# Performance work log

Measured on AMD Instinct MI355X. Metric: run time of the kernel, lower is better.

## Reference

```python
import jax, jax.numpy as jnp
import numpy as np

FRAME_LENGTH = 64
ATTENUATE_GAIN = 0.01


def setup_inputs() -> dict:
    key = jax.random.key(0)
    k1, k2 = jax.random.split(key)
    B, F, FC = 32, 4000, 65
    H = jax.random.uniform(k1, (B, F, FC), dtype=jnp.float32)
    noise = jax.random.uniform(k2, (B, F, FRAME_LENGTH), dtype=jnp.float32)
    return {"H": H, "noise": noise}


def reference(H, noise):
    B, F, fc = H.shape
    M = 2 * fc - 1                      # linear-phase IR length (129)
    L = M + FRAME_LENGTH - 1            # FFT conv length (192)

    # periodic hann window, matching torch.hann_window default
    win = 0.5 * (1.0 - jnp.cos(2.0 * jnp.pi * jnp.arange(M, dtype=jnp.float32) / M))

    # zero-phase FR -> zero-phase IR -> linear-phase windowed IR
    ir = jnp.fft.irfft(H.astype(jnp.complex64), n=M, axis=-1)  # (B, F, M)
    ir = jnp.roll(ir, fc - 1, axis=-1) * win

    # FFT-domain filtering (rfft with n=L zero-pads, same as explicit pad)
    IR = jnp.fft.rfft(ir, n=L, axis=-1)                        # (B, F, L//2+1)
    N = jnp.fft.rfft(noise * 2.0 - 1.0, n=L, axis=-1)          # (B, F, L//2+1)
    X = N * IR

    # Faithful to the original: irfft with n = number of BINS (97), which
    # trims the spectrum to n//2+1 bins and outputs n time samples.
    nb = X.shape[-1]                                           # 97
    y = jnp.fft.irfft(X, n=nb, axis=-1) * ATTENUATE_GAIN       # (B, F, nb)

    # overlap-add (equivalent to conv_transpose1d with identity kernel, stride=frame_length)
    out_len = (F - 1) * FRAME_LENGTH + nb
    idx = jnp.arange(F)[:, None] * FRAME_LENGTH + jnp.arange(nb)[None, :]  # (F, nb)
    out = jnp.zeros((B, out_len), dtype=y.dtype).at[:, idx].add(y)
    return out
```

## Files before the change

### kernel.cpp

```cpp
#include <hip/hip_runtime.h>
#include <math.h>

#define FC     65
#define NB     97
#define FRAME  64
#define B_     32
#define F_     4000
#define OUT_LEN ((F_ - 1) * FRAME + NB)
#define CHUNK  63
#define NCHUNK 64
#define ST     64
#define MROW   160

#define KP     128
#define D_ROW0 0
#define W_ROW0 64
#define E_ROW0 129
#define NROWS  226
#define GUARD_IDX (NROWS * KP)
#define MAGIC  0x5F3C0FEE

__global__ void fn_init(float* __restrict__ ws, int useGuard) {
    if (useGuard && ((const int*)ws)[GUARD_IDX] == MAGIC) return;
    int tid = blockIdx.x * blockDim.x + threadIdx.x;
    if (tid >= NROWS * KP) return;
    int row = tid >> 7;
    int fo  = tid & 127;
    int s   = fo >> 4;
    int w   = fo & 15;
    int slot = w >> 1, im = w & 1;
    int cnt  = (s == 0) ? 7 : 6;
    float val = 0.0f;
    if (slot < cnt) {
        int k = (s == 0) ? slot : (6 * s + 1 + slot);
        if (row < 64) {
            int j = row;
            double x = -(double)(k * j) / 96.0;
            val = im ? (float)sinpi(x) : (float)cospi(x);
        } else if (row < 129) {
            int kap = row - 64;
            double sr_ = cospi(-(double)k / 96.0), si_ = sinpi(-(double)k / 96.0);
            double er = 1.0, ei = 0.0;
            double C2 = 2.0 * cospi(2.0 * (double)kap / 129.0);
            double c_prev = cospi(-130.0 * (double)kap / 129.0);
            double c_cur  = cospi(-128.0 * (double)kap / 129.0);
            double U2 = 2.0 * cospi(2.0 / 129.0);
            double u_prev = cospi(2.0 / 129.0);
            double u_cur  = 1.0;
            double accr = 0.0, acci = 0.0;
            for (int m = 0; m < 129; m++) {
                double win = 0.5 * (1.0 - u_cur);
                double a = win * (1.0 / 129.0);
                if (kap) a *= 2.0 * c_cur;
                accr += a * er; acci += a * ei;
                double un = U2 * u_cur - u_prev; u_prev = u_cur; u_cur = un;
                double cn = C2 * c_cur - c_prev; c_prev = c_cur; c_cur = cn;
                double e2r = er * sr_ - ei * si_;
                double e2i = er * si_ + ei * sr_;
                er = e2r; ei = e2i;
            }
            val = im ? (float)acci : (float)accr;
        } else {
            int t = row - 129;
            double g = 0.01 / 97.0;
            double x = 2.0 * (double)(k * t) / 97.0;
            val = im ? (float)(k == 0 ? 0.0 : -2.0 * g * sinpi(x))
                     : (float)(g * (k == 0 ? 1.0 : 2.0) * cospi(x));
        }
    }
    ws[tid] = val;
}

__global__ void fn_seal(float* __restrict__ ws) { ((int*)ws)[GUARD_IDX] = MAGIC; }

__device__ __forceinline__ float dppx1(float x) {
    return __int_as_float(__builtin_amdgcn_mov_dpp(__float_as_int(x), 0xB1, 0xF, 0xF, false));
}
__device__ __forceinline__ float dppx2(float x) {
    return __int_as_float(__builtin_amdgcn_mov_dpp(__float_as_int(x), 0x4E, 0xF, 0xF, false));
}
__device__ __forceinline__ float dpphm(float x) {
    return __int_as_float(__builtin_amdgcn_mov_dpp(__float_as_int(x), 0x141, 0xF, 0xF, false));
}

#define FR4(M) M(0) M(1) M(2) M(3)

#define DXS(f,s) float Xr##f##_##s = 0.f, Xi##f##_##s = 0.f;
#define DXF(f) DXS(f,0) DXS(f,1) DXS(f,2) DXS(f,3) DXS(f,4) DXS(f,5) DXS(f,6)

#define P1S(f,nf,re,im,s) Xr##f##_##s = fmaf(nf,re,Xr##f##_##s); Xi##f##_##s = fmaf(nf,im,Xi##f##_##s);
#define P1F(f,nf,A,B,C,D) P1S(f,nf,A.x,A.y,0) P1S(f,nf,A.z,A.w,1) P1S(f,nf,B.x,B.y,2) \
  P1S(f,nf,B.z,B.w,3) P1S(f,nf,C.x,C.y,4) P1S(f,nf,C.z,C.w,5) P1S(f,nf,D.x,D.y,6)
#define P1ROW(A,B,C,D,na) P1F(0,na.x,A,B,C,D) P1F(1,na.y,A,B,C,D) P1F(2,na.z,A,B,C,D) P1F(3,na.w,A,B,C,D)

#define P3S(f,hf,re,im,s) Rr##f##_##s = fmaf(hf,re,Rr##f##_##s); Ri##f##_##s = fmaf(hf,im,Ri##f##_##s);
#define P3FA(f,hf,A,B) P3S(f,hf,A.x,A.y,0) P3S(f,hf,A.z,A.w,1) P3S(f,hf,B.x,B.y,2) P3S(f,hf,B.z,B.w,3)
#define P3ROWA(A,B,ha) P3FA(0,ha.x,A,B) P3FA(1,ha.y,A,B) P3FA(2,ha.z,A,B) P3FA(3,ha.w,A,B)
#define P3FB(f,hf,C,D) P3S(f,hf,C.x,C.y,4) P3S(f,hf,C.z,C.w,5) P3S(f,hf,D.x,D.y,6)
#define P3ROWB(C,D,ha) P3FB(0,ha.x,C,D) P3FB(1,ha.y,C,D) P3FB(2,ha.z,C,D) P3FB(3,ha.w,C,D)

#define P4S(f,s) { float xr_ = Xr##f##_##s*Rr##f##_##s - Xi##f##_##s*Ri##f##_##s; \
  Xi##f##_##s = Xr##f##_##s*Ri##f##_##s + Xi##f##_##s*Rr##f##_##s; Xr##f##_##s = xr_; }
#define P4FA(f) P4S(f,0) P4S(f,1) P4S(f,2) P4S(f,3)
#define P4FB(f) P4S(f,4) P4S(f,5) P4S(f,6)

#define P5S(f,re,im,s) y##f = fmaf(Xr##f##_##s,re,y##f); y##f = fmaf(Xi##f##_##s,im,y##f);
#define P5F(f,A,B,C,D) P5S(f,A.x,A.y,0) P5S(f,A.z,A.w,1) P5S(f,B.x,B.y,2) P5S(f,B.z,B.w,3) \
  P5S(f,C.x,C.y,4) P5S(f,C.z,C.w,5) P5S(f,D.x,D.y,6)
#define P5ROW(A,B,C,D) P5F(0,A,B,C,D) P5F(1,A,B,C,D) P5F(2,A,B,C,D) P5F(3,A,B,C,D)

#define P5REDUCE \
    float m0 = y0 + dpphm(y0); \
    float m1 = y1 + dpphm(y1); \
    float m2 = y2 + dpphm(y2); \
    float m3 = y3 + dpphm(y3); \
    float n0, n1, ym; \
    { float a_=(kg&2)?m2:m0, b_=(kg&2)?m0:m2; n0 = a_ + dppx2(b_); } \
    { float a_=(kg&2)?m3:m1, b_=(kg&2)?m1:m3; n1 = a_ + dppx2(b_); } \
    { float a_=(kg&1)?n1:n0, b_=(kg&1)?n0:n1; ym = a_ + dppx1(b_); }

#define OLAH(t_) if (kg < 4 && so) buf[(so - 1) * 65 + (t_)] = ym;
#define OLAT(t_) if (kg < 4) { int rr = (t_) - 64; \
    if (so < 63) buf[so * 65 + rr] += ym; \
    if (isLast) out[lastBase + (t_)] = ym; }

__launch_bounds__(128, 2)
__global__ void fn_main_kernel(const float* __restrict__ H,
                               const float* __restrict__ noise,
                               const float* __restrict__ ws,
                               float* __restrict__ out) {
    __shared__ __align__(16) float buf[65 * ST];
    __shared__ __align__(16) float lmat[4 * MROW];

    int bid = blockIdx.x;
    int b = bid >> 6;
    int c = bid & 63;
    int f0 = c * CHUNK;
    int nf = (CHUNK < F_ - f0) ? CHUNK : (F_ - f0);
    int T  = threadIdx.x;
    int wv = T >> 6;
    int L  = T & 63;
    int kg = L & 7;
    int fs = 32 * wv + 4 * (L >> 3);
    int so = fs + kg;
    int isLast = (kg < 4) && (f0 - 1 + so == F_ - 1);
    long lastBase = (long)b * OUT_LEN + (long)(F_ - 1) * FRAME;

    int srow = T >> 5;
    int sidx = T & 31;
    const float4* wsm = (const float4*)ws;
    float4* lput = (float4*)lmat + srow * 40 + (sidx >> 2) * 5 + (sidx & 3);
    const float4* lget = (const float4*)lmat + kg * 5;

    {
        int slot = T >> 1, half = T & 1;
        long nbase = ((long)b * F_ + (f0 - 1)) * FRAME + (long)slot * FRAME + half * 32;
        const long nmax = (long)B_ * F_ * FRAME - 4;
#pragma unroll 1
        for (int s4 = 0; s4 < 8; s4++) {
            long g = nbase + 4 * s4;
            g = g < 0 ? 0 : (g > nmax ? nmax : g);
            float4 v = *(const float4*)(noise + g);
            float4 w4;
            w4.x = fmaf(2.0f, v.x, -1.0f); w4.y = fmaf(2.0f, v.y, -1.0f);
            w4.z = fmaf(2.0f, v.z, -1.0f); w4.w = fmaf(2.0f, v.w, -1.0f);
            if (c == 0 && slot == 0) { w4.x = w4.y = w4.z = w4.w = 0.0f; }
            int s0 = half * 32 + 4 * s4;
            buf[(s0 + 0) * ST + slot] = w4.x;
            buf[(s0 + 1) * ST + slot] = w4.y;
            buf[(s0 + 2) * ST + slot] = w4.z;
            buf[(s0 + 3) * ST + slot] = w4.w;
        }
    }

    FR4(DXF)

    {
        float4 pf = wsm[(D_ROW0 + srow) * 32 + sidx];
#pragma unroll 1
        for (int g = 0; g < 16; g++) {
            __syncthreads();
            *lput = pf;
            if (g < 15) pf = wsm[(D_ROW0 + 4 * (g + 1) + srow) * 32 + sidx];
            __syncthreads();
#pragma unroll
            for (int r = 0; r < 4; r++) {
                int j = 4 * g + r;
                float4 na = *(const float4*)(buf + j * ST + fs);
                const float4* row4 = lget + r * 40;
                float4 a0 = row4[0], a1 = row4[1], a2 = row4[2], a3 = row4[3];
                P1ROW(a0, a1, a2, a3, na)
            }
        }
    }
    __syncthreads();

    {
        long hbase = ((long)b * F_ + (f0 - 1 + L)) * FC;
        const long hmax = (long)B_ * F_ * FC - 1;
        int k0 = wv ? 33 : 0, k1 = wv ? 65 : 33;
#pragma unroll 1
        for (int kap = k0; kap < k1; kap++) {
            long g = hbase + kap;
            g = g < 0 ? 0 : (g > hmax ? hmax : g);
            buf[kap * ST + L] = H[g];
        }
    }

    {
#define DRFA(f) float Rr##f##_0=0.f,Ri##f##_0=0.f,Rr##f##_1=0.f,Ri##f##_1=0.f, \
                      Rr##f##_2=0.f,Ri##f##_2=0.f,Rr##f##_3=0.f,Ri##f##_3=0.f;
        FR4(DRFA)
#undef DRFA
        float4 pf = wsm[(W_ROW0 + srow) * 32 + sidx];
#pragma unroll 1
        for (int g = 0; g < 17; g++) {
            int cnt = (g == 16) ? 1 : 4;
            __syncthreads();
            if (srow < cnt) *lput = pf;
            { int nr = 4 * (g + 1) + srow; if (nr < 65) pf = wsm[(W_ROW0 + nr) * 32 + sidx]; }
            __syncthreads();
#pragma unroll
            for (int r = 0; r < 4; r++) {
                if (r < cnt) {
                    int kap = 4 * g + r;
                    float4 ha = *(const float4*)(buf + kap * ST + fs);
                    const float4* row4 = lget + r * 40;
                    float4 a0 = row4[0], a1 = row4[1];
                    P3ROWA(a0, a1, ha)
                }
            }
        }
        FR4(P4FA)
    }
    {
#define DRFB(f) float Rr##f##_4=0.f,Ri##f##_4=0.f,Rr##f##_5=0.f,Ri##f##_5=0.f, \
                      Rr##f##_6=0.f,Ri##f##_6=0.f;
        FR4(DRFB)
#undef DRFB
        float4 pf = wsm[(W_ROW0 + srow) * 32 + sidx];
#pragma unroll 1
        for (int g = 0; g < 17; g++) {
            int cnt = (g == 16) ? 1 : 4;
            __syncthreads();
            if (srow < cnt) *lput = pf;
            { int nr = 4 * (g + 1) + srow; if (nr < 65) pf = wsm[(W_ROW0 + nr) * 32 + sidx]; }
            __syncthreads();
#pragma unroll
            for (int r = 0; r < 4; r++) {
                if (r < cnt) {
                    int kap = 4 * g + r;
                    float4 ha = *(const float4*)(buf + kap * ST + fs);
                    const float4* row4 = lget + r * 40;
                    float4 c0 = row4[2], c1 = row4[3];
                    P3ROWB(c0, c1, ha)
                }
            }
        }
        FR4(P4FB)
    }

    {
        float4 pf = wsm[(E_ROW0 + srow) * 32 + sidx];
#pragma unroll 1
        for (int g = 0; g < 16; g++) {
            __syncthreads();
            *lput = pf;
            if (g < 15) pf = wsm[(E_ROW0 + 4 * (g + 1) + srow) * 32 + sidx];
            __syncthreads();
#pragma unroll
            for (int r = 0; r < 4; r++) {
                int t = 4 * g + r;
                const float4* row4 = lget + r * 40;
                float4 a0 = row4[0], a1 = row4[1], a2 = row4[2], a3 = row4[3];
                float y0 = 0.f, y1 = 0.f, y2 = 0.f, y3 = 0.f;
                P5ROW(a0, a1, a2, a3)
                P5REDUCE
                OLAH(t)
            }
        }
    }

    {
        float4 pf = wsm[(E_ROW0 + 64 + srow) * 32 + sidx];
#pragma unroll 1
        for (int g = 0; g < 9; g++) {
            int cnt = (g == 8) ? 1 : 4;
            __syncthreads();
            if (srow < cnt) *lput = pf;
            { int nr = 4 * (g + 1) + srow; if (nr < 33) pf = wsm[(E_ROW0 + 64 + nr) * 32 + sidx]; }
            __syncthreads();
#pragma unroll
            for (int r = 0; r < 4; r++) {
                if (r < cnt) {
                    int t = 64 + 4 * g + r;
                    const float4* row4 = lget + r * 40;
                    float4 a0 = row4[0], a1 = row4[1], a2 = row4[2], a3 = row4[3];
                    float y0 = 0.f, y1 = 0.f, y2 = 0.f, y3 = 0.f;
                    P5ROW(a0, a1, a2, a3)
                    P5REDUCE
                    OLAT(t)
                }
            }
        }
    }
    __syncthreads();

    long obase2 = (long)b * OUT_LEN + (long)f0 * FRAME;
#pragma unroll 1
    for (int i = wv; i < nf; i += 2) {
        out[obase2 + (long)i * 64 + L] = buf[i * 65 + L];
    }
}

extern "C" void kernel_launch(void* const* d_in, const int* in_sizes, int n_in,
                              void* d_out, int out_size, void* d_ws, size_t ws_size,
                              hipStream_t stream) {
    const float* H     = (const float*)d_in[0];
    const float* noise = (const float*)d_in[1];
    float* out = (float*)d_out;
    float* ws  = (float*)d_ws;

    int useGuard = (ws_size >= (size_t)(NROWS * KP + 1) * sizeof(float)) ? 1 : 0;
    fn_init<<<(NROWS * KP + 255) / 256, 256, 0, stream>>>(ws, useGuard);
    fn_main_kernel<<<B_ * NCHUNK, 128, 0, stream>>>(H, noise, ws, out);
    if (useGuard) fn_seal<<<1, 1, 0, stream>>>(ws);
}
```

Measured before the change: 217.7 us.

## Double-buffer DFT matrix staging in LDS with one barrier per group

Replaces the single LDS matrix tile, which needed two barriers per 4-row group, with a double-buffered tile of 3 rows per stage. The next stage is written while the current one is consumed, so each step needs only one __syncthreads. The LDS layout is also padded (35 float4 per row, with a skip every 9) to spread bank accesses. In exchange, 105 of 128 threads do the staging, there are more, smaller groups per phase, and the index math is more involved.

```diff
diff --git a/kernel.cpp b/kernel.cpp
--- a/kernel.cpp
+++ b/kernel.cpp
@@ -10,7 +10,6 @@
 #define CHUNK  63
 #define NCHUNK 64
 #define ST     64
-#define MROW   160
 
 #define KP     128
 #define D_ROW0 0
@@ -19,6 +18,7 @@
 #define NROWS  226
 #define GUARD_IDX (NROWS * KP)
 #define MAGIC  0x5F3C0FEE
+
 
 __global__ void fn_init(float* __restrict__ ws, int useGuard) {
     if (useGuard && ((const int*)ws)[GUARD_IDX] == MAGIC) return;
@@ -124,13 +124,16 @@
     if (so < 63) buf[so * 65 + rr] += ym; \
     if (isLast) out[lastBase + (t_)] = ym; }
 
+#define MSTAGE(rowbase, nrows, gg) { int rr_ = 3 * (gg) + srow; \
+    if (sOn && rr_ < (nrows)) pf = wsm[((rowbase) + rr_) * 32 + g4]; }
+
 __launch_bounds__(128, 2)
 __global__ void fn_main_kernel(const float* __restrict__ H,
                                const float* __restrict__ noise,
                                const float* __restrict__ ws,
                                float* __restrict__ out) {
     __shared__ __align__(16) float buf[65 * ST];
-    __shared__ __align__(16) float lmat[4 * MROW];
+    __shared__ float4 mbuf[2 * 105];
 
     int bid = blockIdx.x;
     int b = bid >> 6;
@@ -146,11 +149,13 @@
     int isLast = (kg < 4) && (f0 - 1 + so == F_ - 1);
     long lastBase = (long)b * OUT_LEN + (long)(F_ - 1) * FRAME;
 
-    int srow = T >> 5;
-    int sidx = T & 31;
+    int srow = T / 35;
+    int si   = T - srow * 35;
+    int sOn  = T < 105;
+    int g4   = si - (si > 8) - (si > 17) - (si > 26);
     const float4* wsm = (const float4*)ws;
-    float4* lput = (float4*)lmat + srow * 40 + (sidx >> 2) * 5 + (sidx & 3);
-    const float4* lget = (const float4*)lmat + kg * 5;
+    int segs4 = 4 * kg + (kg >> 1);
+    float4 pf;
 
     {
         int slot = T >> 1, half = T & 1;
@@ -176,24 +181,29 @@
     FR4(DXF)
 
     {
-        float4 pf = wsm[(D_ROW0 + srow) * 32 + sidx];
-#pragma unroll 1
-        for (int g = 0; g < 16; g++) {
-            __syncthreads();
-            *lput = pf;
-            if (g < 15) pf = wsm[(D_ROW0 + 4 * (g + 1) + srow) * 32 + sidx];
-            __syncthreads();
-#pragma unroll
-            for (int r = 0; r < 4; r++) {
-                int j = 4 * g + r;
+        MSTAGE(D_ROW0, 64, 0)
+        if (sOn) mbuf[T] = pf;
+        MSTAGE(D_ROW0, 64, 1)
+        __syncthreads();
+        int cur = 0;
+#pragma unroll 1
+        for (int g = 0; g < 22; g++) {
+            if (g + 1 < 22) { if (sOn) mbuf[(cur ^ 1) * 105 + T] = pf; }
+            MSTAGE(D_ROW0, 64, g + 2)
+            int cnt = 64 - 3 * g; if (cnt > 3) cnt = 3;
+            const float4* mb = mbuf + cur * 105 + segs4;
+#pragma unroll
+            for (int r = 0; r < 3; r++) if (r < cnt) {
+                int j = 3 * g + r;
                 float4 na = *(const float4*)(buf + j * ST + fs);
-                const float4* row4 = lget + r * 40;
+                const float4* row4 = mb + r * 35;
                 float4 a0 = row4[0], a1 = row4[1], a2 = row4[2], a3 = row4[3];
                 P1ROW(a0, a1, a2, a3, na)
             }
-        }
-    }
-    __syncthreads();
+            __syncthreads();
+            cur ^= 1;
+        }
+    }
 
     {
         long hbase = ((long)b * F_ + (f0 - 1 + L)) * FC;
@@ -212,24 +222,27 @@
                       Rr##f##_2=0.f,Ri##f##_2=0.f,Rr##f##_3=0.f,Ri##f##_3=0.f;
         FR4(DRFA)
 #undef DRFA
-        float4 pf = wsm[(W_ROW0 + srow) * 32 + sidx];
-#pragma unroll 1
-        for (int g = 0; g < 17; g++) {
-            int cnt = (g == 16) ? 1 : 4;
-            __syncthreads();
-            if (srow < cnt) *lput = pf;
-            { int nr = 4 * (g + 1) + srow; if (nr < 65) pf = wsm[(W_ROW0 + nr) * 32 + sidx]; }
-            __syncthreads();
-#pragma unroll
-            for (int r = 0; r < 4; r++) {
-                if (r < cnt) {
-                    int kap = 4 * g + r;
-                    float4 ha = *(const float4*)(buf + kap * ST + fs);
-                    const float4* row4 = lget + r * 40;
-                    float4 a0 = row4[0], a1 = row4[1];
-                    P3ROWA(a0, a1, ha)
-                }
-            }
+        MSTAGE(W_ROW0, 65, 0)
+        if (sOn) mbuf[T] = pf;
+        MSTAGE(W_ROW0, 65, 1)
+        __syncthreads();
+        int cur = 0;
+#pragma unroll 1
+        for (int g = 0; g < 22; g++) {
+            if (g + 1 < 22) { if (sOn) mbuf[(cur ^ 1) * 105 + T] = pf; }
+            MSTAGE(W_ROW0, 65, g + 2)
+            int cnt = 65 - 3 * g; if (cnt > 3) cnt = 3;
+            const float4* mb = mbuf + cur * 105 + segs4;
+#pragma unroll
+            for (int r = 0; r < 3; r++) if (r < cnt) {
+                int kap = 3 * g + r;
+                float4 ha = *(const float4*)(buf + kap * ST + fs);
+                const float4* row4 = mb + r * 35;
+                float4 a0 = row4[0], a1 = row4[1];
+                P3ROWA(a0, a1, ha)
+            }
+            __syncthreads();
+            cur ^= 1;
         }
         FR4(P4FA)
     }
@@ -238,73 +251,84 @@
                       Rr##f##_6=0.f,Ri##f##_6=0.f;
         FR4(DRFB)
 #undef DRFB
-        float4 pf = wsm[(W_ROW0 + srow) * 32 + sidx];
-#pragma unroll 1
-        for (int g = 0; g < 17; g++) {
-            int cnt = (g == 16) ? 1 : 4;
-            __syncthreads();
-            if (srow < cnt) *lput = pf;
-            { int nr = 4 * (g + 1) + srow; if (nr < 65) pf = wsm[(W_ROW0 + nr) * 32 + sidx]; }
-            __syncthreads();
-#pragma unroll
-            for (int r = 0; r < 4; r++) {
-                if (r < cnt) {
-                    int kap = 4 * g + r;
-                    float4 ha = *(const float4*)(buf + kap * ST + fs);
-                    const float4* row4 = lget + r * 40;
-                    float4 c0 = row4[2], c1 = row4[3];
-                    P3ROWB(c0, c1, ha)
-                }
-            }
+        MSTAGE(W_ROW0, 65, 0)
+        if (sOn) mbuf[T] = pf;
+        MSTAGE(W_ROW0, 65, 1)
+        __syncthreads();
+        int cur = 0;
+#pragma unroll 1
+        for (int g = 0; g < 22; g++) {
+            if (g + 1 < 22) { if (sOn) mbuf[(cur ^ 1) * 105 + T] = pf; }
+            MSTAGE(W_ROW0, 65, g + 2)
+            int cnt = 65 - 3 * g; if (cnt > 3) cnt = 3;
+            const float4* mb = mbuf + cur * 105 + segs4;
+#pragma unroll
+            for (int r = 0; r < 3; r++) if (r < cnt) {
+                int kap = 3 * g + r;
+                float4 ha = *(const float4*)(buf + kap * ST + fs);
+                const float4* row4 = mb + r * 35;
+                float4 c0 = row4[2], c1 = row4[3];
+                P3ROWB(c0, c1, ha)
+            }
+            __syncthreads();
+            cur ^= 1;
         }
         FR4(P4FB)
     }
 
     {
-        float4 pf = wsm[(E_ROW0 + srow) * 32 + sidx];
-#pragma unroll 1
-        for (int g = 0; g < 16; g++) {
-            __syncthreads();
-            *lput = pf;
-            if (g < 15) pf = wsm[(E_ROW0 + 4 * (g + 1) + srow) * 32 + sidx];
-            __syncthreads();
-#pragma unroll
-            for (int r = 0; r < 4; r++) {
-                int t = 4 * g + r;
-                const float4* row4 = lget + r * 40;
+        MSTAGE(E_ROW0, 64, 0)
+        if (sOn) mbuf[T] = pf;
+        MSTAGE(E_ROW0, 64, 1)
+        __syncthreads();
+        int cur = 0;
+#pragma unroll 1
+        for (int g = 0; g < 22; g++) {
+            if (g + 1 < 22) { if (sOn) mbuf[(cur ^ 1) * 105 + T] = pf; }
+            MSTAGE(E_ROW0, 64, g + 2)
+            int cnt = 64 - 3 * g; if (cnt > 3) cnt = 3;
+            const float4* mb = mbuf + cur * 105 + segs4;
+#pragma unroll
+            for (int r = 0; r < 3; r++) if (r < cnt) {
+                int t = 3 * g + r;
+                const float4* row4 = mb + r * 35;
                 float4 a0 = row4[0], a1 = row4[1], a2 = row4[2], a3 = row4[3];
                 float y0 = 0.f, y1 = 0.f, y2 = 0.f, y3 = 0.f;
                 P5ROW(a0, a1, a2, a3)
                 P5REDUCE
                 OLAH(t)
             }
-        }
-    }
-
-    {
-        float4 pf = wsm[(E_ROW0 + 64 + srow) * 32 + sidx];
-#pragma unroll 1
-        for (int g = 0; g < 9; g++) {
-            int cnt = (g == 8) ? 1 : 4;
-            __syncthreads();
-            if (srow < cnt) *lput = pf;
-            { int nr = 4 * (g + 1) + srow; if (nr < 33) pf = wsm[(E_ROW0 + 64 + nr) * 32 + sidx]; }
-            __syncthreads();
-#pragma unroll
-            for (int r = 0; r < 4; r++) {
-                if (r < cnt) {
-                    int t = 64 + 4 * g + r;
-                    const float4* row4 = lget + r * 40;
-                    float4 a0 = row4[0], a1 = row4[1], a2 = row4[2], a3 = row4[3];
-                    float y0 = 0.f, y1 = 0.f, y2 = 0.f, y3 = 0.f;
-                    P5ROW(a0, a1, a2, a3)
-                    P5REDUCE
-                    OLAT(t)
-                }
-            }
-        }
-    }
-    __syncthreads();
+            __syncthreads();
+            cur ^= 1;
+        }
+    }
+
+    {
+        MSTAGE(E_ROW0 + 64, 33, 0)
+        if (sOn) mbuf[T] = pf;
+        MSTAGE(E_ROW0 + 64, 33, 1)
+        __syncthreads();
+        int cur = 0;
+#pragma unroll 1
+        for (int g = 0; g < 11; g++) {
+            if (g + 1 < 11) { if (sOn) mbuf[(cur ^ 1) * 105 + T] = pf; }
+            MSTAGE(E_ROW0 + 64, 33, g + 2)
+            int cnt = 33 - 3 * g; if (cnt > 3) cnt = 3;
+            const float4* mb = mbuf + cur * 105 + segs4;
+#pragma unroll
+            for (int r = 0; r < 3; r++) if (r < cnt) {
+                int t = 64 + 3 * g + r;
+                const float4* row4 = mb + r * 35;
+                float4 a0 = row4[0], a1 = row4[1], a2 = row4[2], a3 = row4[3];
+                float y0 = 0.f, y1 = 0.f, y2 = 0.f, y3 = 0.f;
+                P5ROW(a0, a1, a2, a3)
+                P5REDUCE
+                OLAT(t)
+            }
+            __syncthreads();
+            cur ^= 1;
+        }
+    }
 
     long obase2 = (long)b * OUT_LEN + (long)f0 * FRAME;
 #pragma unroll 1
```

After: 237.2 us. 1.09x slower.

## Exploit inverse-DFT symmetry to compute output sample pairs from split cos/sin sums

Applied to the files above, without the earlier changes.

The final inverse-DFT stage now accumulates the cosine and sine parts separately. Each matrix row then yields two time samples, t and 97-t, as sum and difference, which roughly halves the stage-5 row passes and their shared-memory matrix staging. The shared matrix layout is also changed to a 35-float4 stride with gaps, replacing the padded 160-float rows, and the per-group row counts are now computed instead of branched. In exchange the kernel keeps 33 extra tail accumulators in registers and fully unrolls the stage into straight-line code, which raises register pressure and code size.

```diff
diff --git a/kernel.cpp b/kernel.cpp
--- a/kernel.cpp
+++ b/kernel.cpp
@@ -10,7 +10,6 @@
 #define CHUNK  63
 #define NCHUNK 64
 #define ST     64
-#define MROW   160
 
 #define KP     128
 #define D_ROW0 0
@@ -19,6 +18,7 @@
 #define NROWS  226
 #define GUARD_IDX (NROWS * KP)
 #define MAGIC  0x5F3C0FEE
+
 
 __global__ void fn_init(float* __restrict__ ws, int useGuard) {
     if (useGuard && ((const int*)ws)[GUARD_IDX] == MAGIC) return;
@@ -84,6 +84,9 @@
 }
 
 #define FR4(M) M(0) M(1) M(2) M(3)
+#define R33(M) M(0) M(1) M(2) M(3) M(4) M(5) M(6) M(7) M(8) M(9) M(10) M(11) M(12) \
+  M(13) M(14) M(15) M(16) M(17) M(18) M(19) M(20) M(21) M(22) M(23) M(24) M(25) \
+  M(26) M(27) M(28) M(29) M(30) M(31) M(32)
 
 #define DXS(f,s) float Xr##f##_##s = 0.f, Xi##f##_##s = 0.f;
 #define DXF(f) DXS(f,0) DXS(f,1) DXS(f,2) DXS(f,3) DXS(f,4) DXS(f,5) DXS(f,6)
@@ -104,25 +107,57 @@
 #define P4FA(f) P4S(f,0) P4S(f,1) P4S(f,2) P4S(f,3)
 #define P4FB(f) P4S(f,4) P4S(f,5) P4S(f,6)
 
-#define P5S(f,re,im,s) y##f = fmaf(Xr##f##_##s,re,y##f); y##f = fmaf(Xi##f##_##s,im,y##f);
-#define P5F(f,A,B,C,D) P5S(f,A.x,A.y,0) P5S(f,A.z,A.w,1) P5S(f,B.x,B.y,2) P5S(f,B.z,B.w,3) \
-  P5S(f,C.x,C.y,4) P5S(f,C.z,C.w,5) P5S(f,D.x,D.y,6)
-#define P5ROW(A,B,C,D) P5F(0,A,B,C,D) P5F(1,A,B,C,D) P5F(2,A,B,C,D) P5F(3,A,B,C,D)
-
-#define P5REDUCE \
-    float m0 = y0 + dpphm(y0); \
-    float m1 = y1 + dpphm(y1); \
-    float m2 = y2 + dpphm(y2); \
-    float m3 = y3 + dpphm(y3); \
-    float n0, n1, ym; \
-    { float a_=(kg&2)?m2:m0, b_=(kg&2)?m0:m2; n0 = a_ + dppx2(b_); } \
-    { float a_=(kg&2)?m3:m1, b_=(kg&2)?m1:m3; n1 = a_ + dppx2(b_); } \
-    { float a_=(kg&1)?n1:n0, b_=(kg&1)?n0:n1; ym = a_ + dppx1(b_); }
-
-#define OLAH(t_) if (kg < 4 && so) buf[(so - 1) * 65 + (t_)] = ym;
-#define OLAT(t_) if (kg < 4) { int rr = (t_) - 64; \
-    if (so < 63) buf[so * 65 + rr] += ym; \
-    if (isLast) out[lastBase + (t_)] = ym; }
+#define P5CSa(f,VA,VB) yc##f = fmaf(Xr##f##_0,VA.x,yc##f); ys##f = fmaf(Xi##f##_0,VA.y,ys##f); \
+  yc##f = fmaf(Xr##f##_1,VA.z,yc##f); ys##f = fmaf(Xi##f##_1,VA.w,ys##f); \
+  yc##f = fmaf(Xr##f##_2,VB.x,yc##f); ys##f = fmaf(Xi##f##_2,VB.y,ys##f); \
+  yc##f = fmaf(Xr##f##_3,VB.z,yc##f); ys##f = fmaf(Xi##f##_3,VB.w,ys##f);
+#define P5CSb(f,VC,VD) yc##f = fmaf(Xr##f##_4,VC.x,yc##f); ys##f = fmaf(Xi##f##_4,VC.y,ys##f); \
+  yc##f = fmaf(Xr##f##_5,VC.z,yc##f); ys##f = fmaf(Xi##f##_5,VC.w,ys##f); \
+  yc##f = fmaf(Xr##f##_6,VD.x,yc##f); ys##f = fmaf(Xi##f##_6,VD.y,ys##f);
+
+#define P5RED(OUT,a0,a1,a2,a3) { \
+    float m0_ = a0 + dpphm(a0), m1_ = a1 + dpphm(a1); \
+    float m2_ = a2 + dpphm(a2), m3_ = a3 + dpphm(a3); \
+    float p_, q_, n0_, n1_; \
+    p_ = (kg&2)?m2_:m0_; q_ = (kg&2)?m0_:m2_; n0_ = p_ + dppx2(q_); \
+    p_ = (kg&2)?m3_:m1_; q_ = (kg&2)?m1_:m3_; n1_ = p_ + dppx2(q_); \
+    p_ = (kg&1)?n1_:n0_; q_ = (kg&1)?n0_:n1_; OUT = p_ + dppx1(q_); }
+
+#define WH(t_, v_) { if (kg < 4 && so) buf[(so - 1) * 65 + (t_)] = (v_); }
+
+#define PROWCORE(r_) \
+    const float4* row4_ = mbseg + (r_) * 35; \
+    float4 vA_ = row4_[0], vB_ = row4_[1]; \
+    float yc0=0.f,ys0=0.f,yc1=0.f,ys1=0.f,yc2=0.f,ys2=0.f,yc3=0.f,ys3=0.f; \
+    P5CSa(0,vA_,vB_) P5CSa(1,vA_,vB_) P5CSa(2,vA_,vB_) P5CSa(3,vA_,vB_) \
+    vA_ = row4_[2]; vB_ = row4_[3]; \
+    P5CSb(0,vA_,vB_) P5CSb(1,vA_,vB_) P5CSb(2,vA_,vB_) P5CSb(3,vA_,vB_) \
+    float ymc_, yms_; \
+    P5RED(ymc_, yc0,yc1,yc2,yc3) \
+    P5RED(yms_, ys0,ys1,ys2,ys3)
+
+#define PROW0(r_)       { PROWCORE(r_) WH(0, ymc_ + yms_) }
+#define PROWT(r_,t_,c_) { PROWCORE(r_) WH(t_, ymc_ + yms_) ytc##c_ = ymc_ - yms_; }
+#define PROWH(r_,t_,u_) { PROWCORE(r_) WH(t_, ymc_ + yms_) WH(u_, ymc_ - yms_) }
+
+#define DTC(c_) float ytc##c_ = 0.f;
+#define MG(c_) { if (kg < 4) { \
+    if (so < 63) buf[so * 65 + (c_)] += ytc##c_; \
+    if (isLast) out[lastBase + 64 + (c_)] = ytc##c_; } }
+
+#define MLOAD(rowbase, nrows, gg) { \
+    int rrA_ = 4*(gg) + r1; if (rrA_ > (nrows)-1) rrA_ = (nrows)-1; \
+    pfa = wsm[((rowbase) + rrA_) * 32 + g41]; \
+    if (T < 12) { int rrB_ = 4*(gg) + 3; if (rrB_ > (nrows)-1) rrB_ = (nrows)-1; \
+        pfb = wsm[((rowbase) + rrB_) * 32 + g42]; } }
+#define MPUT() { mbuf[T] = pfa; if (T < 12) mbuf[128 + T] = pfb; }
+
+#define P5G(gn, BODY) { \
+    __syncthreads(); \
+    MPUT() \
+    MLOAD(E_ROW0, 97, (gn) + 1) \
+    __syncthreads(); \
+    BODY }
 
 __launch_bounds__(128, 2)
 __global__ void fn_main_kernel(const float* __restrict__ H,
@@ -130,7 +165,7 @@
                                const float* __restrict__ ws,
                                float* __restrict__ out) {
     __shared__ __align__(16) float buf[65 * ST];
-    __shared__ __align__(16) float lmat[4 * MROW];
+    __shared__ float4 mbuf[140];
 
     int bid = blockIdx.x;
     int b = bid >> 6;
@@ -146,11 +181,14 @@
     int isLast = (kg < 4) && (f0 - 1 + so == F_ - 1);
     long lastBase = (long)b * OUT_LEN + (long)(F_ - 1) * FRAME;
 
-    int srow = T >> 5;
-    int sidx = T & 31;
+    int r1 = T / 35, s1 = T - r1 * 35;
+    int g41 = s1 - (s1 > 8) - (s1 > 17) - (s1 > 26);
+    int s2 = 23 + T;
+    int g42 = s2 - 2 - (s2 > 26);
     const float4* wsm = (const float4*)ws;
-    float4* lput = (float4*)lmat + srow * 40 + (sidx >> 2) * 5 + (sidx & 3);
-    const float4* lget = (const float4*)lmat + kg * 5;
+    int segs4 = 4 * kg + (kg >> 1);
+    const float4* mbseg = mbuf + segs4;
+    float4 pfa, pfb;
 
     {
         int slot = T >> 1, half = T & 1;
@@ -176,18 +214,18 @@
     FR4(DXF)
 
     {
-        float4 pf = wsm[(D_ROW0 + srow) * 32 + sidx];
+        MLOAD(D_ROW0, 64, 0)
 #pragma unroll 1
         for (int g = 0; g < 16; g++) {
             __syncthreads();
-            *lput = pf;
-            if (g < 15) pf = wsm[(D_ROW0 + 4 * (g + 1) + srow) * 32 + sidx];
+            MPUT()
+            MLOAD(D_ROW0, 64, g + 1)
             __syncthreads();
 #pragma unroll
             for (int r = 0; r < 4; r++) {
                 int j = 4 * g + r;
                 float4 na = *(const float4*)(buf + j * ST + fs);
-                const float4* row4 = lget + r * 40;
+                const float4* row4 = mbseg + r * 35;
                 float4 a0 = row4[0], a1 = row4[1], a2 = row4[2], a3 = row4[3];
                 P1ROW(a0, a1, a2, a3, na)
             }
@@ -212,23 +250,21 @@
                       Rr##f##_2=0.f,Ri##f##_2=0.f,Rr##f##_3=0.f,Ri##f##_3=0.f;
         FR4(DRFA)
 #undef DRFA
-        float4 pf = wsm[(W_ROW0 + srow) * 32 + sidx];
+        MLOAD(W_ROW0, 65, 0)
 #pragma unroll 1
         for (int g = 0; g < 17; g++) {
-            int cnt = (g == 16) ? 1 : 4;
-            __syncthreads();
-            if (srow < cnt) *lput = pf;
-            { int nr = 4 * (g + 1) + srow; if (nr < 65) pf = wsm[(W_ROW0 + nr) * 32 + sidx]; }
-            __syncthreads();
+            __syncthreads();
+            MPUT()
+            MLOAD(W_ROW0, 65, g + 1)
+            __syncthreads();
+            int cnt = 65 - 4 * g; if (cnt > 4) cnt = 4;
 #pragma unroll
-            for (int r = 0; r < 4; r++) {
-                if (r < cnt) {
-                    int kap = 4 * g + r;
-                    float4 ha = *(const float4*)(buf + kap * ST + fs);
-                    const float4* row4 = lget + r * 40;
-                    float4 a0 = row4[0], a1 = row4[1];
-                    P3ROWA(a0, a1, ha)
-                }
+            for (int r = 0; r < 4; r++) if (r < cnt) {
+                int kap = 4 * g + r;
+                float4 ha = *(const float4*)(buf + kap * ST + fs);
+                const float4* row4 = mbseg + r * 35;
+                float4 a0 = row4[0], a1 = row4[1];
+                P3ROWA(a0, a1, ha)
             }
         }
         FR4(P4FA)
@@ -238,72 +274,44 @@
                       Rr##f##_6=0.f,Ri##f##_6=0.f;
         FR4(DRFB)
 #undef DRFB
-        float4 pf = wsm[(W_ROW0 + srow) * 32 + sidx];
+        MLOAD(W_ROW0, 65, 0)
 #pragma unroll 1
         for (int g = 0; g < 17; g++) {
-            int cnt = (g == 16) ? 1 : 4;
-            __syncthreads();
-            if (srow < cnt) *lput = pf;
-            { int nr = 4 * (g + 1) + srow; if (nr < 65) pf = wsm[(W_ROW0 + nr) * 32 + sidx]; }
-            __syncthreads();
+            __syncthreads();
+            MPUT()
+            MLOAD(W_ROW0, 65, g + 1)
+            __syncthreads();
+            int cnt = 65 - 4 * g; if (cnt > 4) cnt = 4;
 #pragma unroll
-            for (int r = 0; r < 4; r++) {
-                if (r < cnt) {
-                    int kap = 4 * g + r;
-                    float4 ha = *(const float4*)(buf + kap * ST + fs);
-                    const float4* row4 = lget + r * 40;
-                    float4 c0 = row4[2], c1 = row4[3];
-                    P3ROWB(c0, c1, ha)
-                }
+            for (int r = 0; r < 4; r++) if (r < cnt) {
+                int kap = 4 * g + r;
+                float4 ha = *(const float4*)(buf + kap * ST + fs);
+                const float4* row4 = mbseg + r * 35;
+                float4 c0 = row4[2], c1 = row4[3];
+                P3ROWB(c0, c1, ha)
             }
         }
         FR4(P4FB)
     }
 
-    {
-        float4 pf = wsm[(E_ROW0 + srow) * 32 + sidx];
-#pragma unroll 1
-        for (int g = 0; g < 16; g++) {
-            __syncthreads();
-            *lput = pf;
-            if (g < 15) pf = wsm[(E_ROW0 + 4 * (g + 1) + srow) * 32 + sidx];
-            __syncthreads();
-#pragma unroll
-            for (int r = 0; r < 4; r++) {
-                int t = 4 * g + r;
-                const float4* row4 = lget + r * 40;
-                float4 a0 = row4[0], a1 = row4[1], a2 = row4[2], a3 = row4[3];
-                float y0 = 0.f, y1 = 0.f, y2 = 0.f, y3 = 0.f;
-                P5ROW(a0, a1, a2, a3)
-                P5REDUCE
-                OLAH(t)
-            }
-        }
-    }
-
-    {
-        float4 pf = wsm[(E_ROW0 + 64 + srow) * 32 + sidx];
-#pragma unroll 1
-        for (int g = 0; g < 9; g++) {
-            int cnt = (g == 8) ? 1 : 4;
-            __syncthreads();
-            if (srow < cnt) *lput = pf;
-            { int nr = 4 * (g + 1) + srow; if (nr < 33) pf = wsm[(E_ROW0 + 64 + nr) * 32 + sidx]; }
-            __syncthreads();
-#pragma unroll
-            for (int r = 0; r < 4; r++) {
-                if (r < cnt) {
-                    int t = 64 + 4 * g + r;
-                    const float4* row4 = lget + r * 40;
-                    float4 a0 = row4[0], a1 = row4[1], a2 = row4[2], a3 = row4[3];
-                    float y0 = 0.f, y1 = 0.f, y2 = 0.f, y3 = 0.f;
-                    P5ROW(a0, a1, a2, a3)
-                    P5REDUCE
-                    OLAT(t)
-                }
-            }
-        }
-    }
+    R33(DTC)
+    MLOAD(E_ROW0, 97, 0)
+    P5G(0,  PROW0(0)          PROWT(1,1,32)   PROWT(2,2,31)   PROWT(3,3,30))
+    P5G(1,  PROWT(0,4,29)     PROWT(1,5,28)   PROWT(2,6,27)   PROWT(3,7,26))
+    P5G(2,  PROWT(0,8,25)     PROWT(1,9,24)   PROWT(2,10,23)  PROWT(3,11,22))
+    P5G(3,  PROWT(0,12,21)    PROWT(1,13,20)  PROWT(2,14,19)  PROWT(3,15,18))
+    P5G(4,  PROWT(0,16,17)    PROWT(1,17,16)  PROWT(2,18,15)  PROWT(3,19,14))
+    P5G(5,  PROWT(0,20,13)    PROWT(1,21,12)  PROWT(2,22,11)  PROWT(3,23,10))
+    P5G(6,  PROWT(0,24,9)     PROWT(1,25,8)   PROWT(2,26,7)   PROWT(3,27,6))
+    P5G(7,  PROWT(0,28,5)     PROWT(1,29,4)   PROWT(2,30,3)   PROWT(3,31,2))
+    P5G(8,  PROWT(0,32,1)     PROWT(1,33,0)   PROWH(2,34,63)  PROWH(3,35,62))
+    P5G(9,  PROWH(0,36,61)    PROWH(1,37,60)  PROWH(2,38,59)  PROWH(3,39,58))
+    P5G(10, PROWH(0,40,57)    PROWH(1,41,56)  PROWH(2,42,55)  PROWH(3,43,54))
+    P5G(11, PROWH(0,44,53)    PROWH(1,45,52)  PROWH(2,46,51)  PROWH(3,47,50))
+    P5G(12, PROWH(0,48,49))
+    __syncthreads();
+
+    R33(MG)
     __syncthreads();
 
     long obase2 = (long)b * OUT_LEN + (long)f0 * FRAME;
```

Result: no change. 217.3 us (-0.2%).
